# Optimization experiments

Measured on AMD Instinct MI355X. Metric: run time of the kernel, lower is better.

## Reference

```python
import jax, jax.numpy as jnp
import numpy as np

B, F0, D = 4096, 39, 16
CIN = [128, 128, 128]


def setup_inputs() -> dict:
    key = jax.random.key(0)
    ks = jax.random.split(key, 4)
    x = jax.random.normal(ks[0], (B, F0, D), dtype=jnp.float32)
    fields = [F0] + CIN
    inp = {"embedded_features": x}
    for i in range(len(CIN)):
        cin = F0 * fields[i]
        cout = fields[i + 1]
        kw = jax.random.fold_in(ks[1], i)
        # Conv1d default init scale ~ 1/sqrt(fan_in)
        inp[f"W{i}"] = jax.random.normal(kw, (cout, cin), dtype=jnp.float32) / np.sqrt(cin)
        inp[f"b{i}"] = jnp.zeros((cout,), dtype=jnp.float32)
    return inp


def _cin_layer(X0, Xi, W, b):
    # Math identical to: outer_product [B,F0,Fi,D] -> reshape [B,F0*Fi,D] -> 1x1 Conv1d.
    # Conv1d(kernel=1) over the flattened F0*Fi channel dim is a contraction over (j,k):
    #   Xn[b,h,d] = sum_{j,k} W[h, j*Fi+k] * X0[b,j,d] * Xi[b,k,d] + b[h]
    H = W.shape[0]
    F0_, Fi = X0.shape[1], Xi.shape[1]
    Wr = W.reshape(H, F0_, Fi)
    return jnp.einsum('hjk,bjd,bkd->bhd', Wr, X0, Xi) + b[None, :, None]


def reference(embedded_features, W0, b0, W1, b1, W2, b2):
    X0 = embedded_features  # [B, F0, D]
    Ws = [(W0, b0), (W1, b1), (W2, b2)]
    Xi = X0
    res = []
    for W, b in Ws:
        Xi = _cin_layer(X0, Xi, W, b)  # [B, H_i, D]
        res.append(Xi.sum(axis=2))     # sum over embedding dim
    return jnp.concatenate(res, axis=1)  # [B, sum(cin_size)]
```

## Files before the change

kernel.cpp:

```cpp
#include <hip/hip_runtime.h>
#include <stdint.h>


#define NB_F0 39
#define NB_H  128
#define NB_B  4096

typedef float f32x4  __attribute__((ext_vector_type(4)));
typedef float f32x16 __attribute__((ext_vector_type(16)));
typedef short s16x8  __attribute__((ext_vector_type(8)));

__device__ __forceinline__ unsigned short rne_bf16(float f) {
  union { float f; unsigned u; } v; v.f = f;
  return (unsigned short)((v.u + 0x7fffu + ((v.u >> 16) & 1u)) >> 16);
}
__device__ __forceinline__ float bf16_to_f32(unsigned short s) {
  union { unsigned u; float f; } v; v.u = ((unsigned)s) << 16;
  return v.f;
}

__global__ void prep_x0_kernel(const float* __restrict__ X0g,
                               unsigned short* __restrict__ X0T,
                               unsigned short* __restrict__ X0c) {
  const int b = blockIdx.x;
  const int t = threadIdx.x;
  {
    const int d  = t >> 4;
    const int k4 = (t & 15) << 2;
    unsigned short vv[4];
#pragma unroll
    for (int i = 0; i < 4; ++i) {
      const int k = k4 + i;
      vv[i] = (k < NB_F0) ? rne_bf16(X0g[(size_t)b * (NB_F0 * 16) + k * 16 + d])
                          : (unsigned short)0;
    }
    ushort4 pk; pk.x = vv[0]; pk.y = vv[1]; pk.z = vv[2]; pk.w = vv[3];
    *(ushort4*)&X0T[((size_t)b * 16 + d) * 64 + k4] = pk;
  }
  for (int idx = t; idx < NB_F0 * 16; idx += 256) {
    const int j = idx >> 4, pos = idx & 15;
    const int d = (pos & 3) | (((pos >> 3) & 1) << 2) | (((pos >> 2) & 1) << 3);
    X0c[(size_t)b * (NB_F0 * 16) + idx] =
        rne_bf16(X0g[(size_t)b * (NB_F0 * 16) + j * 16 + d]);
  }
}

__global__ void prep_w_kernel(const float* __restrict__ Wsrc,
                              unsigned short* __restrict__ Wdst,
                              int Fi, int kshift, int total) {
  int idx = blockIdx.x * 256 + threadIdx.x;
  if (idx >= total) return;
  const int i    = idx & 7;
  const int lane = (idx >> 3) & 63;
  const int c    = (idx >> 9) & ((1 << kshift) - 1);
  const int jt   = idx >> (9 + kshift);
  const int t    = jt & 3;
  const int j    = jt >> 2;
  const int h = t * 32 + (lane & 31);
  const int k = c * 16 + ((lane >> 5) << 3) + i;
  unsigned short v = 0;
  if (k < Fi) v = rne_bf16(Wsrc[(size_t)h * (NB_F0 * Fi) + j * Fi + k]);
  Wdst[idx] = v;
}

template <int FI_PAD, bool STORE_XN>
__global__ __launch_bounds__(128, 2) void cin_layer(
    const unsigned short* __restrict__ Wf,
    const unsigned short* __restrict__ XiT,
    const unsigned short* __restrict__ X0c,
    const float* __restrict__ bias,
    unsigned short* __restrict__ XnT,
    float* __restrict__ outp)
{
  constexpr int KC16 = FI_PAD / 16;
  constexpr int S    = NB_F0;

  __shared__ __attribute__((aligned(16))) unsigned short x0s[8 * NB_F0 * 16];

  const int tid  = threadIdx.x;
  const int lane = tid & 63;
  const int wv   = tid >> 6;
  const int L    = lane >> 5;
  const int col  = lane & 31;
  const int ht   = blockIdx.x >> 9;
  const int bblk = (blockIdx.x & 511) * 8;
  const int bwave = bblk + wv * 4;

  {
    const unsigned short* src = X0c + (size_t)bblk * (NB_F0 * 16);
    for (int c = tid; c < (8 * NB_F0 * 16) / 8; c += 128)
      *(s16x8*)&x0s[c * 8] = *(const s16x8*)&src[c * 8];
  }

  s16x8 af[2][KC16];
#pragma unroll
  for (int P = 0; P < 2; ++P) {
    const unsigned short* base = XiT +
        ((size_t)(bwave + 2 * P + (col >> 4)) * 16 + (col & 15)) * FI_PAD +
        L * 8;
#pragma unroll
    for (int c = 0; c < KC16; ++c) af[P][c] = *(const s16x8*)(base + c * 16);
  }

  f32x16 Xacc[2], kZero;
#pragma unroll
  for (int r = 0; r < 16; ++r) kZero[r] = 0.f;
#pragma unroll
  for (int P = 0; P < 2; ++P) Xacc[P] = kZero;

  __syncthreads();

  const s16x8* __restrict__ Wf8 = (const s16x8*)Wf;
  auto wload = [&](int j, s16x8 (&w)[KC16]) {
    const s16x8* p = Wf8 + ((size_t)(j * 4 + ht) * KC16) * 64 + lane;
#pragma unroll
    for (int c = 0; c < KC16; ++c) w[c] = p[c * 64];
  };

  const int x0base = (wv * 4) * (NB_F0 * 16) + L * 8;

  auto compute = [&](int s, const s16x8 (&w)[KC16]) {
#pragma unroll
    for (int P = 0; P < 2; ++P) {
      f32x16 y = __builtin_amdgcn_mfma_f32_32x32x16_bf16(af[P][0], w[0],
                                                         kZero, 0, 0, 0);
#pragma unroll
      for (int c = 1; c < KC16; ++c)
        y = __builtin_amdgcn_mfma_f32_32x32x16_bf16(af[P][c], w[c], y, 0, 0, 0);

      const uint4 xu0 = *(const uint4*)
          &x0s[x0base + (2 * P + 0) * (NB_F0 * 16) + s * 16];
      const uint4 xu1 = *(const uint4*)
          &x0s[x0base + (2 * P + 1) * (NB_F0 * 16) + s * 16];
      const unsigned wd[8] = {xu0.x, xu0.y, xu0.z, xu0.w,
                              xu1.x, xu1.y, xu1.z, xu1.w};
      f32x16 xsc;
#pragma unroll
      for (int i = 0; i < 8; ++i) {
        xsc[2 * i]     = __uint_as_float(wd[i] << 16);
        xsc[2 * i + 1] = __uint_as_float(wd[i] & 0xffff0000u);
      }
      Xacc[P] = __builtin_elementwise_fma(xsc, y, Xacc[P]);
    }
  };

  s16x8 wA[KC16], wB[KC16];
  wload(0, wA);
  wload(1, wB);
  int s = 0;
  for (; s + 2 <= S; s += 2) {
    compute(s, wA);
    wload(s + 2 < S ? s + 2 : 0, wA);
    compute(s + 1, wB);
    if (s + 3 < S) wload(s + 3, wB);
  }
  if (s < S) compute(s, wA);

  const float bias_v = bias[ht * 32 + col];
#pragma unroll
  for (int P = 0; P < 2; ++P) {
#pragma unroll
    for (int bh = 0; bh < 2; ++bh) {
      const int b = bwave + 2 * P + bh;
      float v[8];
#pragma unroll
      for (int m = 0; m < 8; ++m) v[m] = Xacc[P][bh * 8 + m] + bias_v;
      if (STORE_XN) {
#pragma unroll
        for (int m = 0; m < 8; ++m) {
          const int d = (m & 3) + 8 * ((m >> 2) & 1) + 4 * L;
          XnT[((size_t)b * 16 + d) * NB_H + ht * 32 + col] = rne_bf16(v[m]);
        }
      }
      float tot = ((v[0] + v[1]) + (v[2] + v[3])) + ((v[4] + v[5]) + (v[6] + v[7]));
      tot += __shfl_xor(tot, 32);
      if (lane < 32) outp[(size_t)b * 384 + ht * 32 + lane] = tot;
    }
  }
}

extern "C" void kernel_launch(void* const* d_in, const int* in_sizes, int n_in,
                              void* d_out, int out_size, void* d_ws, size_t ws_size,
                              hipStream_t stream) {
  (void)in_sizes; (void)n_in; (void)out_size; (void)ws_size;
  const float* X0g = (const float*)d_in[0];
  const float* W0  = (const float*)d_in[1];
  const float* b0  = (const float*)d_in[2];
  const float* W1  = (const float*)d_in[3];
  const float* b1  = (const float*)d_in[4];
  const float* W2  = (const float*)d_in[5];
  const float* b2  = (const float*)d_in[6];
  float* out = (float*)d_out;

  char* p = (char*)d_ws;
  unsigned short* X0T = (unsigned short*)p; p += (size_t)NB_B * 16 * 64 * 2;
  unsigned short* X0c = (unsigned short*)p; p += (size_t)NB_B * NB_F0 * 16 * 2;
  unsigned short* X1T = (unsigned short*)p; p += (size_t)NB_B * 16 * 128 * 2;
  unsigned short* X2T = (unsigned short*)p; p += (size_t)NB_B * 16 * 128 * 2;
  unsigned short* Wf0 = (unsigned short*)p; p += (size_t)NB_F0 * 4 * 4 * 512 * 2;
  unsigned short* Wf1 = (unsigned short*)p; p += (size_t)NB_F0 * 4 * 8 * 512 * 2;
  unsigned short* Wf2 = (unsigned short*)p; p += (size_t)NB_F0 * 4 * 8 * 512 * 2;

  hipLaunchKernelGGL(prep_x0_kernel, dim3(NB_B), dim3(256), 0, stream,
                     X0g, X0T, X0c);
  const int tw0  = NB_F0 * 4 * 4 * 512;
  const int tw12 = NB_F0 * 4 * 8 * 512;
  hipLaunchKernelGGL(prep_w_kernel, dim3((tw0 + 255) / 256), dim3(256), 0, stream,
                     W0, Wf0, 39, 2, tw0);
  hipLaunchKernelGGL(prep_w_kernel, dim3((tw12 + 255) / 256), dim3(256), 0, stream,
                     W1, Wf1, 128, 3, tw12);
  hipLaunchKernelGGL(prep_w_kernel, dim3((tw12 + 255) / 256), dim3(256), 0, stream,
                     W2, Wf2, 128, 3, tw12);

  hipLaunchKernelGGL((cin_layer<64, true>),   dim3(2048), dim3(128), 0, stream,
                     Wf0, X0T, X0c, b0, X1T, out + 0);
  hipLaunchKernelGGL((cin_layer<128, true>),  dim3(2048), dim3(128), 0, stream,
                     Wf1, X1T, X0c, b1, X2T, out + 128);
  hipLaunchKernelGGL((cin_layer<128, false>), dim3(2048), dim3(128), 0, stream,
                     Wf2, X2T, X0c, b2, (unsigned short*)nullptr, out + 256);
}
```

Baseline: 314.2 us.

## Fuse three CIN layers into one kernel with intermediate activations in LDS

Replaces the three per-layer launches with one fused kernel. Each 256-thread block owns 4 batch rows, and each of its 4 waves computes one 32-wide slice of H. The intermediate X1/X2 activations stay in shared memory instead of round-tripping through global memory, and two launches are dropped. In exchange each block now processes only 4 batch rows, so the weight reloads per block double relative to the 8-row tiles, and occupancy falls to one 256-thread block per the launch bounds. Layers also serialize within a block behind barriers.

```diff
diff --git a/kernel.cpp b/kernel.cpp
--- a/kernel.cpp
+++ b/kernel.cpp
@@ -6,17 +6,14 @@
 #define NB_H  128
 #define NB_B  4096
 
-typedef float f32x4  __attribute__((ext_vector_type(4)));
 typedef float f32x16 __attribute__((ext_vector_type(16)));
 typedef short s16x8  __attribute__((ext_vector_type(8)));
+
+template <int N> struct IC { static constexpr int value = N; };
 
 __device__ __forceinline__ unsigned short rne_bf16(float f) {
   union { float f; unsigned u; } v; v.f = f;
   return (unsigned short)((v.u + 0x7fffu + ((v.u >> 16) & 1u)) >> 16);
-}
-__device__ __forceinline__ float bf16_to_f32(unsigned short s) {
-  union { unsigned u; float f; } v; v.u = ((unsigned)s) << 16;
-  return v.f;
 }
 
 __global__ void prep_x0_kernel(const float* __restrict__ X0g,
@@ -63,120 +60,132 @@
   Wdst[idx] = v;
 }
 
-template <int FI_PAD, bool STORE_XN>
-__global__ __launch_bounds__(128, 2) void cin_layer(
-    const unsigned short* __restrict__ Wf,
-    const unsigned short* __restrict__ XiT,
+__global__ __launch_bounds__(256, 1) void cin_fused(
+    const unsigned short* __restrict__ Wf0,
+    const unsigned short* __restrict__ Wf1,
+    const unsigned short* __restrict__ Wf2,
+    const unsigned short* __restrict__ X0T,
     const unsigned short* __restrict__ X0c,
-    const float* __restrict__ bias,
-    unsigned short* __restrict__ XnT,
+    const float* __restrict__ bias0,
+    const float* __restrict__ bias1,
+    const float* __restrict__ bias2,
     float* __restrict__ outp)
 {
-  constexpr int KC16 = FI_PAD / 16;
-  constexpr int S    = NB_F0;
-
-  __shared__ __attribute__((aligned(16))) unsigned short x0s[8 * NB_F0 * 16];
+  __shared__ __attribute__((aligned(16))) unsigned short x0s[4 * NB_F0 * 16];
+  __shared__ __attribute__((aligned(16))) unsigned short Xa[4 * 16 * 128];
+  __shared__ __attribute__((aligned(16))) unsigned short Xb[4 * 16 * 128];
 
   const int tid  = threadIdx.x;
   const int lane = tid & 63;
   const int wv   = tid >> 6;
   const int L    = lane >> 5;
   const int col  = lane & 31;
-  const int ht   = blockIdx.x >> 9;
-  const int bblk = (blockIdx.x & 511) * 8;
-  const int bwave = bblk + wv * 4;
+  const int bblk = blockIdx.x * 4;
 
   {
     const unsigned short* src = X0c + (size_t)bblk * (NB_F0 * 16);
-    for (int c = tid; c < (8 * NB_F0 * 16) / 8; c += 128)
+    for (int c = tid; c < (4 * NB_F0 * 16) / 8; c += 256)
       *(s16x8*)&x0s[c * 8] = *(const s16x8*)&src[c * 8];
   }
-
-  s16x8 af[2][KC16];
-#pragma unroll
-  for (int P = 0; P < 2; ++P) {
-    const unsigned short* base = XiT +
-        ((size_t)(bwave + 2 * P + (col >> 4)) * 16 + (col & 15)) * FI_PAD +
-        L * 8;
-#pragma unroll
-    for (int c = 0; c < KC16; ++c) af[P][c] = *(const s16x8*)(base + c * 16);
-  }
-
-  f32x16 Xacc[2], kZero;
-#pragma unroll
-  for (int r = 0; r < 16; ++r) kZero[r] = 0.f;
-#pragma unroll
-  for (int P = 0; P < 2; ++P) Xacc[P] = kZero;
-
   __syncthreads();
 
-  const s16x8* __restrict__ Wf8 = (const s16x8*)Wf;
-  auto wload = [&](int j, s16x8 (&w)[KC16]) {
-    const s16x8* p = Wf8 + ((size_t)(j * 4 + ht) * KC16) * 64 + lane;
-#pragma unroll
-    for (int c = 0; c < KC16; ++c) w[c] = p[c * 64];
+  const int x0base = L * 8;
+
+  auto layer = [&](auto kc, const unsigned short* __restrict__ Wl,
+                   const unsigned short* af_base, const float* __restrict__ bv,
+                   float* __restrict__ op, unsigned short* xn) {
+    constexpr int KC16 = decltype(kc)::value;
+    constexpr int FI   = KC16 * 16;
+
+    s16x8 af[2][KC16];
+#pragma unroll
+    for (int P = 0; P < 2; ++P) {
+      const unsigned short* base = af_base +
+          (size_t)(2 * P + (col >> 4)) * (16 * FI) + (col & 15) * FI + L * 8;
+#pragma unroll
+      for (int c = 0; c < KC16; ++c) af[P][c] = *(const s16x8*)(base + c * 16);
+    }
+
+    f32x16 Xacc[2], kZero;
+#pragma unroll
+    for (int r = 0; r < 16; ++r) kZero[r] = 0.f;
+#pragma unroll
+    for (int P = 0; P < 2; ++P) Xacc[P] = kZero;
+
+    const s16x8* __restrict__ W8 = (const s16x8*)Wl;
+    auto wload = [&](int j, s16x8 (&w)[KC16]) {
+      const s16x8* p = W8 + ((size_t)(j * 4 + wv) * KC16) * 64 + lane;
+#pragma unroll
+      for (int c = 0; c < KC16; ++c) w[c] = p[c * 64];
+    };
+
+    auto compute = [&](int s, const s16x8 (&w)[KC16]) {
+#pragma unroll
+      for (int P = 0; P < 2; ++P) {
+        f32x16 y = __builtin_amdgcn_mfma_f32_32x32x16_bf16(af[P][0], w[0],
+                                                           kZero, 0, 0, 0);
+#pragma unroll
+        for (int c = 1; c < KC16; ++c)
+          y = __builtin_amdgcn_mfma_f32_32x32x16_bf16(af[P][c], w[c], y,
+                                                      0, 0, 0);
+        const uint4 xu0 = *(const uint4*)
+            &x0s[x0base + (2 * P + 0) * (NB_F0 * 16) + s * 16];
+        const uint4 xu1 = *(const uint4*)
+            &x0s[x0base + (2 * P + 1) * (NB_F0 * 16) + s * 16];
+        const unsigned wd[8] = {xu0.x, xu0.y, xu0.z, xu0.w,
+                                xu1.x, xu1.y, xu1.z, xu1.w};
+        f32x16 xsc;
+#pragma unroll
+        for (int i = 0; i < 8; ++i) {
+          xsc[2 * i]     = __uint_as_float(wd[i] << 16);
+          xsc[2 * i + 1] = __uint_as_float(wd[i] & 0xffff0000u);
+        }
+        Xacc[P] = __builtin_elementwise_fma(xsc, y, Xacc[P]);
+      }
+    };
+
+    s16x8 wA[KC16], wB[KC16];
+    wload(0, wA);
+    wload(1, wB);
+    int s = 0;
+    for (; s + 2 <= NB_F0; s += 2) {
+      compute(s, wA);
+      wload(s + 2 < NB_F0 ? s + 2 : 0, wA);
+      compute(s + 1, wB);
+      if (s + 3 < NB_F0) wload(s + 3, wB);
+    }
+    if (s < NB_F0) compute(s, wA);
+
+    const float bias_v = bv[wv * 32 + col];
+#pragma unroll
+    for (int P = 0; P < 2; ++P) {
+#pragma unroll
+      for (int bh = 0; bh < 2; ++bh) {
+        const int bl = 2 * P + bh;
+        float v[8];
+#pragma unroll
+        for (int m = 0; m < 8; ++m) v[m] = Xacc[P][bh * 8 + m] + bias_v;
+        if (xn) {
+#pragma unroll
+          for (int m = 0; m < 8; ++m) {
+            const int d = (m & 3) + 8 * ((m >> 2) & 1) + 4 * L;
+            xn[(bl * 16 + d) * 128 + wv * 32 + col] = rne_bf16(v[m]);
+          }
+        }
+        float tot = ((v[0] + v[1]) + (v[2] + v[3])) +
+                    ((v[4] + v[5]) + (v[6] + v[7]));
+        tot += __shfl_xor(tot, 32);
+        if (lane < 32) op[(size_t)(bblk + bl) * 384 + wv * 32 + lane] = tot;
+      }
+    }
   };
 
-  const int x0base = (wv * 4) * (NB_F0 * 16) + L * 8;
-
-  auto compute = [&](int s, const s16x8 (&w)[KC16]) {
-#pragma unroll
-    for (int P = 0; P < 2; ++P) {
-      f32x16 y = __builtin_amdgcn_mfma_f32_32x32x16_bf16(af[P][0], w[0],
-                                                         kZero, 0, 0, 0);
-#pragma unroll
-      for (int c = 1; c < KC16; ++c)
-        y = __builtin_amdgcn_mfma_f32_32x32x16_bf16(af[P][c], w[c], y, 0, 0, 0);
-
-      const uint4 xu0 = *(const uint4*)
-          &x0s[x0base + (2 * P + 0) * (NB_F0 * 16) + s * 16];
-      const uint4 xu1 = *(const uint4*)
-          &x0s[x0base + (2 * P + 1) * (NB_F0 * 16) + s * 16];
-      const unsigned wd[8] = {xu0.x, xu0.y, xu0.z, xu0.w,
-                              xu1.x, xu1.y, xu1.z, xu1.w};
-      f32x16 xsc;
-#pragma unroll
-      for (int i = 0; i < 8; ++i) {
-        xsc[2 * i]     = __uint_as_float(wd[i] << 16);
-        xsc[2 * i + 1] = __uint_as_float(wd[i] & 0xffff0000u);
-      }
-      Xacc[P] = __builtin_elementwise_fma(xsc, y, Xacc[P]);
-    }
-  };
-
-  s16x8 wA[KC16], wB[KC16];
-  wload(0, wA);
-  wload(1, wB);
-  int s = 0;
-  for (; s + 2 <= S; s += 2) {
-    compute(s, wA);
-    wload(s + 2 < S ? s + 2 : 0, wA);
-    compute(s + 1, wB);
-    if (s + 3 < S) wload(s + 3, wB);
-  }
-  if (s < S) compute(s, wA);
-
-  const float bias_v = bias[ht * 32 + col];
-#pragma unroll
-  for (int P = 0; P < 2; ++P) {
-#pragma unroll
-    for (int bh = 0; bh < 2; ++bh) {
-      const int b = bwave + 2 * P + bh;
-      float v[8];
-#pragma unroll
-      for (int m = 0; m < 8; ++m) v[m] = Xacc[P][bh * 8 + m] + bias_v;
-      if (STORE_XN) {
-#pragma unroll
-        for (int m = 0; m < 8; ++m) {
-          const int d = (m & 3) + 8 * ((m >> 2) & 1) + 4 * L;
-          XnT[((size_t)b * 16 + d) * NB_H + ht * 32 + col] = rne_bf16(v[m]);
-        }
-      }
-      float tot = ((v[0] + v[1]) + (v[2] + v[3])) + ((v[4] + v[5]) + (v[6] + v[7]));
-      tot += __shfl_xor(tot, 32);
-      if (lane < 32) outp[(size_t)b * 384 + ht * 32 + lane] = tot;
-    }
-  }
+  layer(IC<4>{}, Wf0, X0T + (size_t)bblk * (16 * 64), bias0, outp + 0,   Xa);
+  __syncthreads();
+  layer(IC<8>{}, Wf1, Xa,                             bias1, outp + 128, Xb);
+  __syncthreads();
+  layer(IC<8>{}, Wf2, Xb,                             bias2, outp + 256,
+        (unsigned short*)nullptr);
 }
 
 extern "C" void kernel_launch(void* const* d_in, const int* in_sizes, int n_in,
@@ -195,8 +204,6 @@
   char* p = (char*)d_ws;
   unsigned short* X0T = (unsigned short*)p; p += (size_t)NB_B * 16 * 64 * 2;
   unsigned short* X0c = (unsigned short*)p; p += (size_t)NB_B * NB_F0 * 16 * 2;
-  unsigned short* X1T = (unsigned short*)p; p += (size_t)NB_B * 16 * 128 * 2;
-  unsigned short* X2T = (unsigned short*)p; p += (size_t)NB_B * 16 * 128 * 2;
   unsigned short* Wf0 = (unsigned short*)p; p += (size_t)NB_F0 * 4 * 4 * 512 * 2;
   unsigned short* Wf1 = (unsigned short*)p; p += (size_t)NB_F0 * 4 * 8 * 512 * 2;
   unsigned short* Wf2 = (unsigned short*)p; p += (size_t)NB_F0 * 4 * 8 * 512 * 2;
@@ -212,10 +219,6 @@
   hipLaunchKernelGGL(prep_w_kernel, dim3((tw12 + 255) / 256), dim3(256), 0, stream,
                      W2, Wf2, 128, 3, tw12);
 
-  hipLaunchKernelGGL((cin_layer<64, true>),   dim3(2048), dim3(128), 0, stream,
-                     Wf0, X0T, X0c, b0, X1T, out + 0);
-  hipLaunchKernelGGL((cin_layer<128, true>),  dim3(2048), dim3(128), 0, stream,
-                     Wf1, X1T, X0c, b1, X2T, out + 128);
-  hipLaunchKernelGGL((cin_layer<128, false>), dim3(2048), dim3(128), 0, stream,
-                     Wf2, X2T, X0c, b2, (unsigned short*)nullptr, out + 256);
-}
+  hipLaunchKernelGGL(cin_fused, dim3(NB_B / 4), dim3(256), 0, stream,
+                     Wf0, Wf1, Wf2, X0T, X0c, b0, b1, b2, out);
+}
```

Result: no change. 308.1 us (-1.9%).
